# Performance work log

Measured on AMD Instinct MI355X. Metric: run time of the kernel, lower is better.

The kernel has to match this reference:

```python
import jax, jax.numpy as jnp
import numpy as np

N = 262144  # number of points
W = 256     # feature width


def setup_inputs() -> dict:
    key = jax.random.key(0)
    k1, k2, k3 = jax.random.split(key, 3)
    x = jax.random.normal(k1, (N, W), dtype=jnp.float32)
    # torch nn.Linear(W, 9) layout: weight [out, in], bias [out]
    fc_w = jax.random.normal(k2, (9, W), dtype=jnp.float32) * (1.0 / np.sqrt(W))
    fc_b = jax.random.normal(k3, (9,), dtype=jnp.float32) * 0.01
    return {"x": x, "fc_w": fc_w, "fc_b": fc_b}


def symmetric_orthogonalization(m):
    # m: [n, 3, 3] -> nearest rotation matrix (special orthogonal Procrustes)
    u, s, vt = jnp.linalg.svd(m, full_matrices=False)
    det = jnp.linalg.det(jnp.einsum('nij,njk->nik', u, vt))  # [n]
    ones = jnp.ones_like(det)
    d = jnp.stack([ones, ones, det], axis=-1)  # [n, 3] diag(1, 1, det)
    r = jnp.einsum('nij,nj,njk->nik', u, d, vt)
    return r


def reference(x, fc_w, fc_b):
    # x: [N, W] -> rotations flattened to [N, 9] (out_type='mat', out_rots=1)
    y = x @ fc_w.T + fc_b            # [N, 9]
    m = y.reshape(-1, 3, 3)          # [N, 3, 3]
    r = symmetric_orthogonalization(m)
    return r.reshape(x.shape[:-1] + (9,))
```

## Files before the change

kernel.cpp:

```cpp
#include <hip/hip_runtime.h>
#include <math.h>

#define N_PTS 262144
#define WIDTH 256

__device__ __forceinline__ void jrot(double &app, double &aqq, double &apq,
                                     double &arp, double &arq,
                                     double &vp0, double &vq0,
                                     double &vp1, double &vq1,
                                     double &vp2, double &vq2)
{
    double a = apq;
    if (fabs(a) < 1e-300) return;
    double theta = (aqq - app) / (2.0 * a);
    double tt = copysign(1.0, theta) / (fabs(theta) + sqrt(1.0 + theta * theta));
    double c = 1.0 / sqrt(1.0 + tt * tt);
    double s = tt * c;
    app -= tt * a;
    aqq += tt * a;
    apq = 0.0;
    double rp = arp, rq = arq;
    arp = c * rp - s * rq;
    arq = s * rp + c * rq;
    double t0p = vp0, t0q = vq0; vp0 = c * t0p - s * t0q; vq0 = s * t0p + c * t0q;
    double t1p = vp1, t1q = vq1; vp1 = c * t1p - s * t1q; vq1 = s * t1p + c * t1q;
    double t2p = vp2, t2q = vq2; vp2 = c * t2p - s * t2q; vq2 = s * t2p + c * t2q;
}

__global__ __launch_bounds__(256) void so3_kernel(
    const float* __restrict__ x,
    const float* __restrict__ fw,
    const float* __restrict__ fb,
    float* __restrict__ out)
{
    __shared__ float xs[256][33];
    const int t  = threadIdx.x;
    const int p0 = blockIdx.x << 8;

    float y[9];
#pragma unroll
    for (int j = 0; j < 9; ++j) y[j] = 0.f;

    for (int kc = 0; kc < 8; ++kc) {
        const int k0 = kc << 5;
#pragma unroll
        for (int i = 0; i < 8; ++i) {
            const int flat = (i << 8) + t;
            const int row  = flat >> 3;
            const int c4   = flat & 7;
            const float4 v = *reinterpret_cast<const float4*>(
                x + (size_t)(p0 + row) * WIDTH + k0 + (c4 << 2));
            xs[row][(c4 << 2) + 0] = v.x;
            xs[row][(c4 << 2) + 1] = v.y;
            xs[row][(c4 << 2) + 2] = v.z;
            xs[row][(c4 << 2) + 3] = v.w;
        }
        __syncthreads();
#pragma unroll
        for (int kk = 0; kk < 32; ++kk) {
            const float xv = xs[t][kk];
            const int k = k0 + kk;
#pragma unroll
            for (int j = 0; j < 9; ++j)
                y[j] = fmaf(xv, fw[j * WIDTH + k], y[j]);
        }
        __syncthreads();
    }
#pragma unroll
    for (int j = 0; j < 9; ++j) y[j] += fb[j];

    const double m00 = y[0], m01 = y[1], m02 = y[2];
    const double m10 = y[3], m11 = y[4], m12 = y[5];
    const double m20 = y[6], m21 = y[7], m22 = y[8];

    double a00 = m00*m00 + m10*m10 + m20*m20;
    double a01 = m00*m01 + m10*m11 + m20*m21;
    double a02 = m00*m02 + m10*m12 + m20*m22;
    double a11 = m01*m01 + m11*m11 + m21*m21;
    double a12 = m01*m02 + m11*m12 + m21*m22;
    double a22 = m02*m02 + m12*m12 + m22*m22;

    double v[3][3] = { {1,0,0}, {0,1,0}, {0,0,1} };

#pragma unroll
    for (int sw = 0; sw < 4; ++sw) {
        jrot(a00, a11, a01, a02, a12,
             v[0][0], v[0][1], v[1][0], v[1][1], v[2][0], v[2][1]);
        jrot(a00, a22, a02, a01, a12,
             v[0][0], v[0][2], v[1][0], v[1][2], v[2][0], v[2][2]);
        jrot(a11, a22, a12, a01, a02,
             v[0][1], v[0][2], v[1][1], v[1][2], v[2][1], v[2][2]);
    }

    double d0 = a00, d1 = a11, d2 = a22, tmp;
    if (d0 < d1) { tmp=d0; d0=d1; d1=tmp;
        tmp=v[0][0]; v[0][0]=v[0][1]; v[0][1]=tmp;
        tmp=v[1][0]; v[1][0]=v[1][1]; v[1][1]=tmp;
        tmp=v[2][0]; v[2][0]=v[2][1]; v[2][1]=tmp; }
    if (d0 < d2) { tmp=d0; d0=d2; d2=tmp;
        tmp=v[0][0]; v[0][0]=v[0][2]; v[0][2]=tmp;
        tmp=v[1][0]; v[1][0]=v[1][2]; v[1][2]=tmp;
        tmp=v[2][0]; v[2][0]=v[2][2]; v[2][2]=tmp; }
    if (d1 < d2) { tmp=d1; d1=d2; d2=tmp;
        tmp=v[0][1]; v[0][1]=v[0][2]; v[0][2]=tmp;
        tmp=v[1][1]; v[1][1]=v[1][2]; v[1][2]=tmp;
        tmp=v[2][1]; v[2][1]=v[2][2]; v[2][2]=tmp; }

    const double v1x = v[0][0], v1y = v[1][0], v1z = v[2][0];
    const double v2x = v[0][1], v2y = v[1][1], v2z = v[2][1];

    double u1x = m00*v1x + m01*v1y + m02*v1z;
    double u1y = m10*v1x + m11*v1y + m12*v1z;
    double u1z = m20*v1x + m21*v1y + m22*v1z;
    double inv1 = 1.0 / (sqrt(u1x*u1x + u1y*u1y + u1z*u1z) + 1e-300);
    u1x *= inv1; u1y *= inv1; u1z *= inv1;

    double u2x = m00*v2x + m01*v2y + m02*v2z;
    double u2y = m10*v2x + m11*v2y + m12*v2z;
    double u2z = m20*v2x + m21*v2y + m22*v2z;
    const double d12 = u1x*u2x + u1y*u2y + u1z*u2z;
    u2x -= d12*u1x; u2y -= d12*u1y; u2z -= d12*u1z;
    double inv2 = 1.0 / (sqrt(u2x*u2x + u2y*u2y + u2z*u2z) + 1e-300);
    u2x *= inv2; u2y *= inv2; u2z *= inv2;

    const double u3x = u1y*u2z - u1z*u2y;
    const double u3y = u1z*u2x - u1x*u2z;
    const double u3z = u1x*u2y - u1y*u2x;
    const double v3x = v1y*v2z - v1z*v2y;
    const double v3y = v1z*v2x - v1x*v2z;
    const double v3z = v1x*v2y - v1y*v2x;

    float r[9];
    r[0] = (float)(u1x*v1x + u2x*v2x + u3x*v3x);
    r[1] = (float)(u1x*v1y + u2x*v2y + u3x*v3y);
    r[2] = (float)(u1x*v1z + u2x*v2z + u3x*v3z);
    r[3] = (float)(u1y*v1x + u2y*v2x + u3y*v3x);
    r[4] = (float)(u1y*v1y + u2y*v2y + u3y*v3y);
    r[5] = (float)(u1y*v1z + u2y*v2z + u3y*v3z);
    r[6] = (float)(u1z*v1x + u2z*v2x + u3z*v3x);
    r[7] = (float)(u1z*v1y + u2z*v2y + u3z*v3y);
    r[8] = (float)(u1z*v1z + u2z*v2z + u3z*v3z);

    float* o = out + (size_t)(p0 + t) * 9;
#pragma unroll
    for (int j = 0; j < 9; ++j) o[j] = r[j];
}

extern "C" void kernel_launch(void* const* d_in, const int* in_sizes, int n_in,
                              void* d_out, int out_size, void* d_ws, size_t ws_size,
                              hipStream_t stream) {
    const float* x  = (const float*)d_in[0];
    const float* fw = (const float*)d_in[1];
    const float* fb = (const float*)d_in[2];
    float* out = (float*)d_out;
    dim3 grid(N_PTS / 256), block(256);
    hipLaunchKernelGGL(so3_kernel, grid, block, 0, stream, x, fw, fb, out);
}
```

Measured before the change: 74.45 us.

## Split fused GEMV and SVD into two kernels via workspace

```diff
diff --git a/kernel.cpp b/kernel.cpp
--- a/kernel.cpp
+++ b/kernel.cpp
@@ -3,6 +3,55 @@
 
 #define N_PTS 262144
 #define WIDTH 256
+
+
+__global__ __launch_bounds__(256, 8) void gemv_kernel(
+    const float* __restrict__ x,
+    const float* __restrict__ fw,
+    const float* __restrict__ fb,
+    float* __restrict__ yws)
+{
+    __shared__ float xs[256][20];
+    const int t  = threadIdx.x;
+    const int p0 = blockIdx.x << 8;
+
+    float y[9];
+#pragma unroll
+    for (int j = 0; j < 9; ++j) y[j] = 0.f;
+
+    for (int kc = 0; kc < 16; ++kc) {
+        const int k0 = kc << 4;
+#pragma unroll
+        for (int i = 0; i < 4; ++i) {
+            const int flat = (i << 8) + t;
+            const int row  = flat >> 2;
+            const int c4   = flat & 3;
+            const float4 v = *reinterpret_cast<const float4*>(
+                x + (size_t)(p0 + row) * WIDTH + k0 + (c4 << 2));
+            *reinterpret_cast<float4*>(&xs[row][c4 << 2]) = v;
+        }
+        __syncthreads();
+#pragma unroll
+        for (int q = 0; q < 4; ++q) {
+            const float4 xv = *reinterpret_cast<const float4*>(&xs[t][q << 2]);
+            const float xa[4] = {xv.x, xv.y, xv.z, xv.w};
+#pragma unroll
+            for (int c = 0; c < 4; ++c) {
+                const int k = k0 + (q << 2) + c;
+#pragma unroll
+                for (int j = 0; j < 9; ++j)
+                    y[j] = fmaf(xa[c], fw[j * WIDTH + k], y[j]);
+            }
+        }
+        __syncthreads();
+    }
+
+    const int p = p0 + t;
+#pragma unroll
+    for (int j = 0; j < 9; ++j)
+        yws[(size_t)j * N_PTS + p] = y[j] + fb[j];
+}
+
 
 __device__ __forceinline__ void jrot(double &app, double &aqq, double &apq,
                                      double &arp, double &arq,
@@ -27,47 +76,16 @@
     double t2p = vp2, t2q = vq2; vp2 = c * t2p - s * t2q; vq2 = s * t2p + c * t2q;
 }
 
-__global__ __launch_bounds__(256) void so3_kernel(
-    const float* __restrict__ x,
-    const float* __restrict__ fw,
-    const float* __restrict__ fb,
+__global__ __launch_bounds__(256) void svd_kernel(
+    const float* __restrict__ yws,
     float* __restrict__ out)
 {
-    __shared__ float xs[256][33];
-    const int t  = threadIdx.x;
-    const int p0 = blockIdx.x << 8;
+    const int p = (blockIdx.x << 8) + threadIdx.x;
 
     float y[9];
 #pragma unroll
-    for (int j = 0; j < 9; ++j) y[j] = 0.f;
-
-    for (int kc = 0; kc < 8; ++kc) {
-        const int k0 = kc << 5;
-#pragma unroll
-        for (int i = 0; i < 8; ++i) {
-            const int flat = (i << 8) + t;
-            const int row  = flat >> 3;
-            const int c4   = flat & 7;
-            const float4 v = *reinterpret_cast<const float4*>(
-                x + (size_t)(p0 + row) * WIDTH + k0 + (c4 << 2));
-            xs[row][(c4 << 2) + 0] = v.x;
-            xs[row][(c4 << 2) + 1] = v.y;
-            xs[row][(c4 << 2) + 2] = v.z;
-            xs[row][(c4 << 2) + 3] = v.w;
-        }
-        __syncthreads();
-#pragma unroll
-        for (int kk = 0; kk < 32; ++kk) {
-            const float xv = xs[t][kk];
-            const int k = k0 + kk;
-#pragma unroll
-            for (int j = 0; j < 9; ++j)
-                y[j] = fmaf(xv, fw[j * WIDTH + k], y[j]);
-        }
-        __syncthreads();
-    }
-#pragma unroll
-    for (int j = 0; j < 9; ++j) y[j] += fb[j];
+    for (int j = 0; j < 9; ++j)
+        y[j] = yws[(size_t)j * N_PTS + p];
 
     const double m00 = y[0], m01 = y[1], m02 = y[2];
     const double m10 = y[3], m11 = y[4], m12 = y[5];
@@ -141,7 +159,7 @@
     r[7] = (float)(u1z*v1y + u2z*v2y + u3z*v3y);
     r[8] = (float)(u1z*v1z + u2z*v2z + u3z*v3z);
 
-    float* o = out + (size_t)(p0 + t) * 9;
+    float* o = out + (size_t)p * 9;
 #pragma unroll
     for (int j = 0; j < 9; ++j) o[j] = r[j];
 }
@@ -153,6 +171,9 @@
     const float* fw = (const float*)d_in[1];
     const float* fb = (const float*)d_in[2];
     float* out = (float*)d_out;
+    float* yws = (float*)d_ws;
+
     dim3 grid(N_PTS / 256), block(256);
-    hipLaunchKernelGGL(so3_kernel, grid, block, 0, stream, x, fw, fb, out);
+    hipLaunchKernelGGL(gemv_kernel, grid, block, 0, stream, x, fw, fb, yws);
+    hipLaunchKernelGGL(svd_kernel,  grid, block, 0, stream, yws, out);
 }
```

After: 95.54 us. 1.28x slower.
